# Kernel tuning notes

Hardware: AMD Instinct MI355X
Metric: run time of the kernel (lower is better)

Reference implementation:

```python
import jax, jax.numpy as jnp
import numpy as np

NUM_ITERATIONS = 3
EPS = 1e-12


def _squash(s):
    # s: (..., V). squash(s) = |s|^2 * s / ((1+|s|^2) * |s|)
    sq = jnp.sum(s * s, axis=-1, keepdims=True)
    return sq * s / ((1.0 + sq) * jnp.sqrt(sq))


def setup_inputs() -> dict:
    key = jax.random.key(0)
    kx, kw = jax.random.split(key)
    B, L, P, V, Q = 16, 64, 1024, 64, 16
    x = jax.random.normal(kx, (B, P, Q), dtype=jnp.float32)
    W = 0.01 * jax.random.normal(kw, (L, P, V, Q), dtype=jnp.float32)
    return {"x": x, "W": W}


def reference(x, W):
    # u_hat[b,l,p,v] = sum_q W[l,p,v,q] * x[b,p,q]
    u_hat = jnp.einsum('lpvq,bpq->blpv', W, x)  # (B, L, P, V)
    B, L, P, V = u_hat.shape
    b_ij = jnp.zeros((B, L, P), dtype=u_hat.dtype)
    c_ij = None
    v = None
    for it in range(NUM_ITERATIONS):  # small fixed unroll
        c_ij = jax.nn.softmax(b_ij, axis=1)  # softmax over latent caps
        s = jnp.einsum('blp,blpv->blv', c_ij, u_hat)
        v = _squash(s)  # (B, L, V)
        if it < NUM_ITERATIONS - 1:
            # agreement update: b_ij += <v_j, u_hat>
            b_ij = b_ij + jnp.einsum('blv,blpv->blp', v, u_hat)
    # T-score: coupling entropy over latent axis, per primary capsule
    cT = jnp.swapaxes(c_ij, 1, 2)  # (B, P, L)
    entropy = -jnp.sum(cT * jnp.log(cT + EPS), axis=-1)  # (B, P)
    T = jnp.mean(1.0 - entropy / np.log(float(L)))
    # D-score: max over caps of population std (over batch) of activation norms
    v_norm = jnp.linalg.norm(v, axis=-1)  # (B, L)
    D = jnp.max(jnp.std(v_norm, axis=0))
    return v, T, D
```

## Files before the change

kernel.cpp:

```cpp
#include <hip/hip_runtime.h>
#include <hip/hip_bf16.h>

#define B 16
#define L 64
#define P 1024
#define V 64
#define Q 16
#define LN64 4.158883083359672f

#define CHBC 16
#define NCH_BC (P / CHBC)

typedef unsigned short ushort8_t __attribute__((ext_vector_type(8)));
typedef __attribute__((ext_vector_type(8))) short bf16x8;
typedef __attribute__((ext_vector_type(4))) float f32x4;

typedef const __attribute__((address_space(1))) void* gld_gptr_t;
typedef __attribute__((address_space(3))) void* gld_lptr_t;

static __device__ __forceinline__ float bf2f(ushort u) {
    return __uint_as_float(((unsigned int)u) << 16);
}
static __device__ __forceinline__ ushort f2bf(float f) {
    unsigned int x = __float_as_uint(f);
    unsigned int r = (x + 0x7fffu + ((x >> 16) & 1u)) >> 16;
    return (ushort)r;
}
static __device__ __forceinline__ unsigned pk2(float lo, float hi) {
    return (unsigned)f2bf(lo) | ((unsigned)f2bf(hi) << 16);
}

static __device__ __forceinline__ float wsum64(float v) {
#pragma unroll
    for (int m = 32; m > 0; m >>= 1) v += __shfl_xor(v, m, 64);
    return v;
}
static __device__ __forceinline__ float wmax64(float v) {
#pragma unroll
    for (int m = 32; m > 0; m >>= 1) v = fmaxf(v, __shfl_xor(v, m, 64));
    return v;
}

union FragU { uint4 u; bf16x8 s; };

__global__ __launch_bounds__(256, 3) void k_uhat(const float* __restrict__ Wt,
                                                 const float* __restrict__ x,
                                                 ushort* __restrict__ uhat,
                                                 float* __restrict__ sp0) {
    const int t = threadIdx.x;
    const int w = t >> 6;
    const int lane = t & 63;
    const int kb = lane >> 4;
    const int cc = lane & 15;
    const int ch = blockIdx.x;
    const int l = blockIdx.y;
    const int p0 = ch * 32;

    __shared__ __align__(16) char smem[49152];
    unsigned int* xstage = (unsigned int*)smem;

#pragma unroll
    for (int i = 0; i < 16; ++i) {
        const int e = i * 256 + t;
        const int pp = e >> 7, ln = (e >> 2) & 31, m = e & 3;
        const int b = ln & 15, qb = (ln >> 4) * 8;
        const float2 xv = *reinterpret_cast<const float2*>(
            x + ((size_t)b * P + p0 + pp) * Q + qb + 2 * m);
        xstage[e] = pk2(xv.x, xv.y);
    }
    __syncthreads();

    uint4 af[8];
#pragma unroll
    for (int i = 0; i < 8; ++i) {
        if (lane < 32)
            af[i] = *reinterpret_cast<const uint4*>(
                smem + ((size_t)(w * 8 + i) * 32 + lane) * 16);
        else
            af[i] = (uint4){0u, 0u, 0u, 0u};
    }
    __syncthreads();

    char* ring = smem + w * 12288;
    const int sperm = (lane & ~3) | ((lane & 3) ^ ((lane >> 3) & 3));
    const char* gW = (const char*)(Wt + ((size_t)l * P + p0 + w * 8) * (V * Q))
                     + (size_t)sperm * 16;
    const int xk = (cc >> 1) & 3;

    f32x4 cacc0 = {0.f, 0.f, 0.f, 0.f}, cacc1 = {0.f, 0.f, 0.f, 0.f};
    f32x4 cacc2 = {0.f, 0.f, 0.f, 0.f}, cacc3 = {0.f, 0.f, 0.f, 0.f};

#define STAGE(i_)                                                             \
    {                                                                         \
        const char* s_ = gW + (size_t)(i_) * 4096;                            \
        char* d_ = ring + ((i_) % 3) * 4096;                                  \
        __builtin_amdgcn_global_load_lds((gld_gptr_t)(s_ + 0),                \
                                         (gld_lptr_t)(d_ + 0), 16, 0, 0);     \
        __builtin_amdgcn_global_load_lds((gld_gptr_t)(s_ + 1024),             \
                                         (gld_lptr_t)(d_ + 1024), 16, 0, 0);  \
        __builtin_amdgcn_global_load_lds((gld_gptr_t)(s_ + 2048),             \
                                         (gld_lptr_t)(d_ + 2048), 16, 0, 0);  \
        __builtin_amdgcn_global_load_lds((gld_gptr_t)(s_ + 3072),             \
                                         (gld_lptr_t)(d_ + 3072), 16, 0, 0);  \
    }

#define WFRAG(g_, dst_)                                                       \
    {                                                                         \
        if (lane < 32) {                                                      \
            const char* rb_ = ring + (slot_) * 4096 + (cc + 16 * (g_)) * 64;  \
            const float4 f0 =                                                 \
                *(const float4*)(rb_ + (((2 * kb + 0) ^ xk) << 4));           \
            const float4 f1 =                                                 \
                *(const float4*)(rb_ + (((2 * kb + 1) ^ xk) << 4));           \
            dst_.u = (uint4){pk2(f0.x, f0.y), pk2(f0.z, f0.w),                \
                             pk2(f1.x, f1.y), pk2(f1.z, f1.w)};               \
        } else {                                                              \
            dst_.u = (uint4){0u, 0u, 0u, 0u};                                 \
        }                                                                     \
    }

#define MMG(g_, cacc_, u_)                                                    \
    {                                                                         \
        FragU wf_;                                                            \
        WFRAG(g_, wf_);                                                       \
        f32x4 d_ = __builtin_amdgcn_mfma_f32_16x16x32_bf16(wf_.s, bx_.s,      \
                                                           cacc_, 0, 0, 0);   \
        u_ = d_ - cacc_;                                                      \
        cacc_ = d_;                                                           \
    }

#define COMPUTE(i_)                                                           \
    {                                                                         \
        const int slot_ = (i_) % 3;                                           \
        const int p_ = p0 + w * 8 + (i_);                                     \
        FragU bx_; bx_.u = af[i_];                                            \
        f32x4 u0_, u1_, u2_, u3_;                                             \
        MMG(0, cacc0, u0_);                                                   \
        MMG(1, cacc1, u1_);                                                   \
        MMG(2, cacc2, u2_);                                                   \
        MMG(3, cacc3, u3_);                                                   \
        uint4 A_, B_;                                                         \
        A_.x = pk2(u0_[0], u1_[0]); A_.y = pk2(u2_[0], u3_[0]);               \
        A_.z = pk2(u0_[1], u1_[1]); A_.w = pk2(u2_[1], u3_[1]);               \
        B_.x = pk2(u0_[2], u1_[2]); B_.y = pk2(u2_[2], u3_[2]);               \
        B_.z = pk2(u0_[3], u1_[3]); B_.w = pk2(u2_[3], u3_[3]);               \
        ushort* ub_ = uhat + (((size_t)l * P + p_) * B + cc) * V + kb * 16;   \
        *reinterpret_cast<uint4*>(ub_) = A_;                                  \
        *reinterpret_cast<uint4*>(ub_ + 8) = B_;                              \
    }

#define WAITV(N)                                                              \
    asm volatile("s_waitcnt vmcnt(" #N ")" ::: "memory");                     \
    __builtin_amdgcn_sched_barrier(0);

    STAGE(0); STAGE(1);
    WAITV(2); STAGE(2); COMPUTE(0);
    WAITV(4); STAGE(3); COMPUTE(1);
    WAITV(6); STAGE(4); COMPUTE(2);
    WAITV(6); STAGE(5); COMPUTE(3);
    WAITV(6); STAGE(6); COMPUTE(4);
    WAITV(6); STAGE(7); COMPUTE(5);
    WAITV(6); COMPUTE(6);
    WAITV(2); COMPUTE(7);

    {
        float* sb = sp0 + (((size_t)l * 128 + ch * 4 + w) * 16 + cc) * 64 + kb * 16;
        float4 q0 = {cacc0[0], cacc1[0], cacc2[0], cacc3[0]};
        float4 q1 = {cacc0[1], cacc1[1], cacc2[1], cacc3[1]};
        float4 q2 = {cacc0[2], cacc1[2], cacc2[2], cacc3[2]};
        float4 q3 = {cacc0[3], cacc1[3], cacc2[3], cacc3[3]};
        *reinterpret_cast<float4*>(sb + 0) = q0;
        *reinterpret_cast<float4*>(sb + 4) = q1;
        *reinterpret_cast<float4*>(sb + 8) = q2;
        *reinterpret_cast<float4*>(sb + 12) = q3;
    }
#undef STAGE
#undef WFRAG
#undef MMG
#undef COMPUTE
#undef WAITV
}

__global__ __launch_bounds__(256) void k_v(const float* __restrict__ sp,
                                           size_t cb, size_t cl, size_t cs,
                                           int nch, float scale, int unperm,
                                           float* __restrict__ vout,
                                           float* __restrict__ norms) {
    const int b = blockIdx.y;
    const int w = threadIdx.x >> 6, lane = threadIdx.x & 63;
    const int l = blockIdx.x * 4 + w;
    const float* p = sp + cb * b + cl * l + lane;
    float s = 0.f;
#pragma unroll 8
    for (int ch = 0; ch < nch; ++ch) s += p[(size_t)ch * cs];
    s *= scale;
    float sq = wsum64(s * s);
    float f = sqrtf(sq) / (1.0f + sq);
    const int vi = unperm ? ((lane & 3) * 16 + (lane >> 4) * 4 + ((lane >> 2) & 3))
                          : lane;
    vout[((size_t)b * L + l) * V + vi] = s * f;
    if (norms && lane == 0) norms[b * L + l] = sq / (1.0f + sq);
}

__global__ __launch_bounds__(512, 4) void k_bc(const ushort* __restrict__ uhat,
                                               const float* __restrict__ vv,
                                               float* __restrict__ bbuf,
                                               float* __restrict__ sp,
                                               float* __restrict__ Tsum,
                                               int add_prev, int do_T) {
    const int ch = blockIdx.x, b = blockIdx.y;
    const int p0 = ch * CHBC;
    const int t = threadIdx.x;
    const int w = t >> 6, lane = t & 63;
    const int pl8 = lane >> 3;
    const int vg8 = lane & 7;
    const int l0 = w * 8;

    __shared__ float vsh[L][V];
    __shared__ float bl[CHBC][L + 1];
    __shared__ float twv[8];

    {
        const float4* vvp = reinterpret_cast<const float4*>(vv + (size_t)b * L * V);
        float4* vshp = reinterpret_cast<float4*>(&vsh[0][0]);
#pragma unroll
        for (int i = 0; i < 2; ++i) vshp[t + i * 512] = vvp[t + i * 512];
    }

    const size_t LSTR = (size_t)P * B * V;
    ushort8_t ur[8][2];
    {
        const ushort* ubase = uhat + (((size_t)l0 * P + p0 + pl8) * B + b) * V + vg8 * 8;
#pragma unroll
        for (int li = 0; li < 8; ++li) {
#pragma unroll
            for (int ph = 0; ph < 2; ++ph)
                ur[li][ph] = *reinterpret_cast<const ushort8_t*>(
                    ubase + (size_t)li * LSTR + (size_t)ph * 8 * B * V);
        }
    }
    __syncthreads();

#pragma unroll
    for (int li = 0; li < 8; ++li) {
        const int l = l0 + li;
        const float4 va = *reinterpret_cast<const float4*>(&vsh[l][vg8 * 8]);
        const float4 vb = *reinterpret_cast<const float4*>(&vsh[l][vg8 * 8 + 4]);
#pragma unroll
        for (int ph = 0; ph < 2; ++ph) {
            float d;
            d = bf2f(ur[li][ph][0]) * va.x;
            d = fmaf(bf2f(ur[li][ph][1]), va.y, d);
            d = fmaf(bf2f(ur[li][ph][2]), va.z, d);
            d = fmaf(bf2f(ur[li][ph][3]), va.w, d);
            d = fmaf(bf2f(ur[li][ph][4]), vb.x, d);
            d = fmaf(bf2f(ur[li][ph][5]), vb.y, d);
            d = fmaf(bf2f(ur[li][ph][6]), vb.z, d);
            d = fmaf(bf2f(ur[li][ph][7]), vb.w, d);
            d += __shfl_xor(d, 1, 64);
            d += __shfl_xor(d, 2, 64);
            d += __shfl_xor(d, 4, 64);
            if (vg8 == 0) bl[ph * 8 + pl8][l] = d;
        }
    }
    __syncthreads();

    float tloc = 0.f;
#pragma unroll
    for (int pi = 0; pi < 2; ++pi) {
        const int pli = w * 2 + pi;
        const int p = p0 + pli;
        float bv = bl[pli][lane];
        float* bp = bbuf + ((size_t)b * P + p) * L;
        if (add_prev) bv += bp[lane];
        bp[lane] = bv;
        float m = wmax64(bv);
        float e = __expf(bv - m);
        float ssum = wsum64(e);
        float cc = e / ssum;
        bl[pli][lane] = cc;
        if (do_T) tloc += cc * __logf(64.0f * (cc + 1e-12f));
    }
    if (do_T) {
        float dsum = wsum64(tloc);
        if (lane == 0) twv[w] = dsum;
    }
    __syncthreads();
    if (do_T && t == 0) {
        float s8 = twv[0] + twv[1] + twv[2] + twv[3] +
                   twv[4] + twv[5] + twv[6] + twv[7];
        atomicAdd(Tsum, s8 * (1.0f / LN64));
    }

    float* spb = sp + (size_t)(b * NCH_BC + ch) * L * V;
#pragma unroll
    for (int li = 0; li < 8; ++li) {
        const int l = l0 + li;
        const float cA = bl[pl8][l];
        const float cB = bl[8 + pl8][l];
        float4 pa, pb;
        pa.x = cA * bf2f(ur[li][0][0]) + cB * bf2f(ur[li][1][0]);
        pa.y = cA * bf2f(ur[li][0][1]) + cB * bf2f(ur[li][1][1]);
        pa.z = cA * bf2f(ur[li][0][2]) + cB * bf2f(ur[li][1][2]);
        pa.w = cA * bf2f(ur[li][0][3]) + cB * bf2f(ur[li][1][3]);
        pb.x = cA * bf2f(ur[li][0][4]) + cB * bf2f(ur[li][1][4]);
        pb.y = cA * bf2f(ur[li][0][5]) + cB * bf2f(ur[li][1][5]);
        pb.z = cA * bf2f(ur[li][0][6]) + cB * bf2f(ur[li][1][6]);
        pb.w = cA * bf2f(ur[li][0][7]) + cB * bf2f(ur[li][1][7]);
#pragma unroll
        for (int m = 8; m <= 32; m <<= 1) {
            pa.x += __shfl_xor(pa.x, m, 64);
            pa.y += __shfl_xor(pa.y, m, 64);
            pa.z += __shfl_xor(pa.z, m, 64);
            pa.w += __shfl_xor(pa.w, m, 64);
            pb.x += __shfl_xor(pb.x, m, 64);
            pb.y += __shfl_xor(pb.y, m, 64);
            pb.z += __shfl_xor(pb.z, m, 64);
            pb.w += __shfl_xor(pb.w, m, 64);
        }
        if (pl8 == 0) {
            *reinterpret_cast<float4*>(spb + (size_t)l * V + vg8 * 8) = pa;
            *reinterpret_cast<float4*>(spb + (size_t)l * V + vg8 * 8 + 4) = pb;
        }
    }
}

__global__ void k_final(const float* __restrict__ Tsum,
                        const float* __restrict__ norms,
                        float* __restrict__ out) {
    const int lane = threadIdx.x & 63;
    float n[B];
    float sum = 0.f;
#pragma unroll
    for (int b = 0; b < B; ++b) { n[b] = norms[b * L + lane]; sum += n[b]; }
    const float mean = sum * (1.0f / B);
    float var = 0.f;
#pragma unroll
    for (int b = 0; b < B; ++b) { float d = n[b] - mean; var = fmaf(d, d, var); }
    var *= (1.0f / B);
    float sd = sqrtf(var);
    float D = wmax64(sd);
    if (lane == 0) {
        out[B * L * V] = Tsum[0] * (1.0f / (B * P));
        out[B * L * V + 1] = D;
    }
}

extern "C" void kernel_launch(void* const* d_in, const int* in_sizes, int n_in,
                              void* d_out, int out_size, void* d_ws, size_t ws_size,
                              hipStream_t stream) {
    const float* x = (const float*)d_in[0];
    const float* W = (const float*)d_in[1];
    float* out = (float*)d_out;

    char* ws = (char*)d_ws;
    ushort* uhat = (ushort*)ws;
    size_t off = (size_t)B * L * P * V * 2;
    float* spbuf = (float*)(ws + off);
    off += (size_t)64 * 128 * 16 * 64 * 4;
    float* vbuf  = (float*)(ws + off); off += (size_t)B * L * V * 4;
    float* bbuf  = (float*)(ws + off); off += (size_t)B * P * L * 4;
    float* norms = (float*)(ws + off); off += (size_t)B * L * 4;
    float* Tsum  = (float*)(ws + off); off += 256;

    hipMemsetAsync(Tsum, 0, sizeof(float), stream);

    hipLaunchKernelGGL(k_uhat, dim3(32, 64), dim3(256), 0, stream, W, x, uhat, spbuf);
    hipLaunchKernelGGL(k_v, dim3(L / 4, B), dim3(256), 0, stream,
                       spbuf, (size_t)64, (size_t)131072, (size_t)1024, 128,
                       1.0f / 64.0f, 0, vbuf, (float*)nullptr);
    hipLaunchKernelGGL(k_bc, dim3(NCH_BC, B), dim3(512), 0, stream,
                       uhat, vbuf, bbuf, spbuf, Tsum, 0, 0);
    hipLaunchKernelGGL(k_v, dim3(L / 4, B), dim3(256), 0, stream,
                       spbuf, (size_t)NCH_BC * L * V, (size_t)V, (size_t)L * V,
                       NCH_BC, 1.0f, 0, vbuf, (float*)nullptr);
    hipLaunchKernelGGL(k_bc, dim3(NCH_BC, B), dim3(512), 0, stream,
                       uhat, vbuf, bbuf, spbuf, Tsum, 1, 1);
    hipLaunchKernelGGL(k_v, dim3(L / 4, B), dim3(256), 0, stream,
                       spbuf, (size_t)NCH_BC * L * V, (size_t)V, (size_t)L * V,
                       NCH_BC, 1.0f, 1, out, norms);
    hipLaunchKernelGGL(k_final, dim3(1), dim3(64), 0, stream, Tsum, norms, out);
}
```

Measured before the change: 220.4 us.

## Load W directly into registers and process primary capsule pairs per MFMA

Drops the LDS ring of global_load_lds transfers for W and instead loads W fp32 values straight into registers with a two-slot register double buffer. Each W fragment now serves two primary capsules: the even capsule's x goes in lanes 0-31 and the odd capsule's x in lanes 32-63, which uses the previously zeroed half of the lanes. The aim is to cut LDS round-trips and the k-padding waste. The cost is higher register pressure and possibly less coalesced global loads.

```diff
diff --git a/kernel.cpp b/kernel.cpp
--- a/kernel.cpp
+++ b/kernel.cpp
@@ -14,9 +14,6 @@
 typedef unsigned short ushort8_t __attribute__((ext_vector_type(8)));
 typedef __attribute__((ext_vector_type(8))) short bf16x8;
 typedef __attribute__((ext_vector_type(4))) float f32x4;
-
-typedef const __attribute__((address_space(1))) void* gld_gptr_t;
-typedef __attribute__((address_space(3))) void* gld_lptr_t;
 
 static __device__ __forceinline__ float bf2f(ushort u) {
     return __uint_as_float(((unsigned int)u) << 16);
@@ -56,8 +53,7 @@
     const int l = blockIdx.y;
     const int p0 = ch * 32;
 
-    __shared__ __align__(16) char smem[49152];
-    unsigned int* xstage = (unsigned int*)smem;
+    __shared__ unsigned int xstage[32][32][4];
 
 #pragma unroll
     for (int i = 0; i < 16; ++i) {
@@ -66,102 +62,92 @@
         const int b = ln & 15, qb = (ln >> 4) * 8;
         const float2 xv = *reinterpret_cast<const float2*>(
             x + ((size_t)b * P + p0 + pp) * Q + qb + 2 * m);
-        xstage[e] = pk2(xv.x, xv.y);
+        xstage[pp][ln][m] = pk2(xv.x, xv.y);
     }
     __syncthreads();
 
-    uint4 af[8];
-#pragma unroll
-    for (int i = 0; i < 8; ++i) {
+    uint4 afe[4], afo[4];
+#pragma unroll
+    for (int i = 0; i < 4; ++i) {
         if (lane < 32)
-            af[i] = *reinterpret_cast<const uint4*>(
-                smem + ((size_t)(w * 8 + i) * 32 + lane) * 16);
+            afe[i] = *reinterpret_cast<const uint4*>(&xstage[w * 8 + 2 * i][lane][0]);
         else
-            af[i] = (uint4){0u, 0u, 0u, 0u};
-    }
-    __syncthreads();
-
-    char* ring = smem + w * 12288;
-    const int sperm = (lane & ~3) | ((lane & 3) ^ ((lane >> 3) & 3));
-    const char* gW = (const char*)(Wt + ((size_t)l * P + p0 + w * 8) * (V * Q))
-                     + (size_t)sperm * 16;
-    const int xk = (cc >> 1) & 3;
+            afe[i] = (uint4){0u, 0u, 0u, 0u};
+        if (lane >= 32)
+            afo[i] = *reinterpret_cast<const uint4*>(&xstage[w * 8 + 2 * i + 1][lane - 32][0]);
+        else
+            afo[i] = (uint4){0u, 0u, 0u, 0u};
+    }
+
+    const float* gW = Wt + ((size_t)l * P + p0 + w * 8) * (V * Q);
+    const float* lb = gW + (size_t)(kb >> 1) * (V * Q) + cc * Q + (kb & 1) * 8;
 
     f32x4 cacc0 = {0.f, 0.f, 0.f, 0.f}, cacc1 = {0.f, 0.f, 0.f, 0.f};
     f32x4 cacc2 = {0.f, 0.f, 0.f, 0.f}, cacc3 = {0.f, 0.f, 0.f, 0.f};
-
-#define STAGE(i_)                                                             \
+    float4 wl[2][8];
+
+#define LOADP(i_, s_)                                                         \
     {                                                                         \
-        const char* s_ = gW + (size_t)(i_) * 4096;                            \
-        char* d_ = ring + ((i_) % 3) * 4096;                                  \
-        __builtin_amdgcn_global_load_lds((gld_gptr_t)(s_ + 0),                \
-                                         (gld_lptr_t)(d_ + 0), 16, 0, 0);     \
-        __builtin_amdgcn_global_load_lds((gld_gptr_t)(s_ + 1024),             \
-                                         (gld_lptr_t)(d_ + 1024), 16, 0, 0);  \
-        __builtin_amdgcn_global_load_lds((gld_gptr_t)(s_ + 2048),             \
-                                         (gld_lptr_t)(d_ + 2048), 16, 0, 0);  \
-        __builtin_amdgcn_global_load_lds((gld_gptr_t)(s_ + 3072),             \
-                                         (gld_lptr_t)(d_ + 3072), 16, 0, 0);  \
-    }
-
-#define WFRAG(g_, dst_)                                                       \
-    {                                                                         \
-        if (lane < 32) {                                                      \
-            const char* rb_ = ring + (slot_) * 4096 + (cc + 16 * (g_)) * 64;  \
-            const float4 f0 =                                                 \
-                *(const float4*)(rb_ + (((2 * kb + 0) ^ xk) << 4));           \
-            const float4 f1 =                                                 \
-                *(const float4*)(rb_ + (((2 * kb + 1) ^ xk) << 4));           \
-            dst_.u = (uint4){pk2(f0.x, f0.y), pk2(f0.z, f0.w),                \
-                             pk2(f1.x, f1.y), pk2(f1.z, f1.w)};               \
-        } else {                                                              \
-            dst_.u = (uint4){0u, 0u, 0u, 0u};                                 \
+        const float* bp_ = lb + (size_t)(2 * (i_)) * (V * Q);                 \
+        _Pragma("unroll")                                                     \
+        for (int g_ = 0; g_ < 4; ++g_) {                                      \
+            wl[s_][2 * g_ + 0] = *(const float4*)(bp_ + g_ * 256);            \
+            wl[s_][2 * g_ + 1] = *(const float4*)(bp_ + g_ * 256 + 4);        \
         }                                                                     \
     }
 
-#define MMG(g_, cacc_, u_)                                                    \
+#define ONEG(g_, s_, cacc_, ue_, uo_)                                         \
     {                                                                         \
         FragU wf_;                                                            \
-        WFRAG(g_, wf_);                                                       \
-        f32x4 d_ = __builtin_amdgcn_mfma_f32_16x16x32_bf16(wf_.s, bx_.s,      \
-                                                           cacc_, 0, 0, 0);   \
-        u_ = d_ - cacc_;                                                      \
-        cacc_ = d_;                                                           \
-    }
-
-#define COMPUTE(i_)                                                           \
+        const float4 f0_ = wl[s_][2 * g_ + 0];                                \
+        const float4 f1_ = wl[s_][2 * g_ + 1];                                \
+        wf_.u = (uint4){pk2(f0_.x, f0_.y), pk2(f0_.z, f0_.w),                 \
+                        pk2(f1_.x, f1_.y), pk2(f1_.z, f1_.w)};                \
+        f32x4 De_ = __builtin_amdgcn_mfma_f32_16x16x32_bf16(wf_.s, axe_.s,    \
+                                                            cacc_, 0, 0, 0);  \
+        ue_ = De_ - cacc_;                                                    \
+        f32x4 Do_ = __builtin_amdgcn_mfma_f32_16x16x32_bf16(wf_.s, axo_.s,    \
+                                                            De_, 0, 0, 0);    \
+        uo_ = Do_ - De_;                                                      \
+        cacc_ = Do_;                                                          \
+    }
+
+#define STOREU(u0_, u1_, u2_, u3_, p_)                                        \
     {                                                                         \
-        const int slot_ = (i_) % 3;                                           \
-        const int p_ = p0 + w * 8 + (i_);                                     \
-        FragU bx_; bx_.u = af[i_];                                            \
-        f32x4 u0_, u1_, u2_, u3_;                                             \
-        MMG(0, cacc0, u0_);                                                   \
-        MMG(1, cacc1, u1_);                                                   \
-        MMG(2, cacc2, u2_);                                                   \
-        MMG(3, cacc3, u3_);                                                   \
-        uint4 A_, B_;                                                         \
+        uint4 A_, Bv_;                                                        \
         A_.x = pk2(u0_[0], u1_[0]); A_.y = pk2(u2_[0], u3_[0]);               \
         A_.z = pk2(u0_[1], u1_[1]); A_.w = pk2(u2_[1], u3_[1]);               \
-        B_.x = pk2(u0_[2], u1_[2]); B_.y = pk2(u2_[2], u3_[2]);               \
-        B_.z = pk2(u0_[3], u1_[3]); B_.w = pk2(u2_[3], u3_[3]);               \
-        ushort* ub_ = uhat + (((size_t)l * P + p_) * B + cc) * V + kb * 16;   \
+        Bv_.x = pk2(u0_[2], u1_[2]); Bv_.y = pk2(u2_[2], u3_[2]);             \
+        Bv_.z = pk2(u0_[3], u1_[3]); Bv_.w = pk2(u2_[3], u3_[3]);             \
+        ushort* ub_ = uhat + (((size_t)l * P + (p_)) * B + cc) * V + kb * 16; \
         *reinterpret_cast<uint4*>(ub_) = A_;                                  \
-        *reinterpret_cast<uint4*>(ub_ + 8) = B_;                              \
+        *reinterpret_cast<uint4*>(ub_ + 8) = Bv_;                             \
+    }
+
+#define COMPUTEP(i_, s_)                                                      \
+    {                                                                         \
+        FragU axe_; axe_.u = afe[i_];                                         \
+        FragU axo_; axo_.u = afo[i_];                                         \
+        f32x4 ue0_, ue1_, ue2_, ue3_, uo0_, uo1_, uo2_, uo3_;                 \
+        ONEG(0, s_, cacc0, ue0_, uo0_);                                       \
+        ONEG(1, s_, cacc1, ue1_, uo1_);                                       \
+        ONEG(2, s_, cacc2, ue2_, uo2_);                                       \
+        ONEG(3, s_, cacc3, ue3_, uo3_);                                       \
+        const int pe_ = p0 + w * 8 + 2 * (i_);                                \
+        STOREU(ue0_, ue1_, ue2_, ue3_, pe_);                                  \
+        STOREU(uo0_, uo1_, uo2_, uo3_, pe_ + 1);                              \
     }
 
 #define WAITV(N)                                                              \
     asm volatile("s_waitcnt vmcnt(" #N ")" ::: "memory");                     \
     __builtin_amdgcn_sched_barrier(0);
 
-    STAGE(0); STAGE(1);
-    WAITV(2); STAGE(2); COMPUTE(0);
-    WAITV(4); STAGE(3); COMPUTE(1);
-    WAITV(6); STAGE(4); COMPUTE(2);
-    WAITV(6); STAGE(5); COMPUTE(3);
-    WAITV(6); STAGE(6); COMPUTE(4);
-    WAITV(6); STAGE(7); COMPUTE(5);
-    WAITV(6); COMPUTE(6);
-    WAITV(2); COMPUTE(7);
+    LOADP(0, 0);
+    LOADP(1, 1);
+    WAITV(8);  COMPUTEP(0, 0); LOADP(2, 0);
+    WAITV(12); COMPUTEP(1, 1); LOADP(3, 1);
+    WAITV(12); COMPUTEP(2, 0);
+    WAITV(4);  COMPUTEP(3, 1);
 
     {
         float* sb = sp0 + (((size_t)l * 128 + ch * 4 + w) * 16 + cc) * 64 + kb * 16;
@@ -174,10 +160,10 @@
         *reinterpret_cast<float4*>(sb + 8) = q2;
         *reinterpret_cast<float4*>(sb + 12) = q3;
     }
-#undef STAGE
-#undef WFRAG
-#undef MMG
-#undef COMPUTE
+#undef LOADP
+#undef ONEG
+#undef STOREU
+#undef COMPUTEP
 #undef WAITV
 }
 
```

New measurement: 222.4 us. Within noise of the previous version (+0.9%).
